# Kernel tuning notes

Hardware: AMD Instinct MI355X
Metric: run time of the kernel (lower is better)

The kernel has to match this reference:

```python
import jax, jax.numpy as jnp
import numpy as np

D = 64          # internal token dim (patch_encoder output)
E = 4           # num_experts
HID = 256       # expert hidden dim
NCLS = 10       # classifier output (hardcoded in source)


def gelu(x):
    return jax.nn.gelu(x, approximate=False)  # torch nn.GELU default = exact erf


def setup_inputs() -> dict:
    key = jax.random.key(0)
    ks = jax.random.split(key, 16)
    B, S, IN = 128, 1024, 192
    sc = lambda k, sh, fan: (jax.random.normal(k, sh, jnp.float32) / np.sqrt(fan))
    return {
        "x": jax.random.normal(ks[0], (B, S, IN), jnp.float32),
        # patch encoder: Linear(IN,64) -> GELU -> Linear(64,D)
        "pe_w1": sc(ks[1], (IN, 64), IN), "pe_b1": jnp.zeros((64,), jnp.float32),
        "pe_w2": sc(ks[2], (64, D), 64),  "pe_b2": jnp.zeros((D,), jnp.float32),
        # gate: Linear(D, E)
        "gate_w": sc(ks[3], (D, E), D), "gate_b": jnp.zeros((E,), jnp.float32),
        # experts: per-expert MLP D -> HID -> D
        "ew1": sc(ks[4], (E, D, HID), D), "eb1": jnp.zeros((E, HID), jnp.float32),
        "ew2": sc(ks[5], (E, HID, D), HID), "eb2": jnp.zeros((E, D), jnp.float32),
        # classifier: LayerNorm(D) -> Linear(D,D) -> GELU -> Linear(D,10)
        "ln_g": jnp.ones((D,), jnp.float32), "ln_b": jnp.zeros((D,), jnp.float32),
        "cl_w1": sc(ks[6], (D, D), D), "cl_b1": jnp.zeros((D,), jnp.float32),
        "cl_w2": sc(ks[7], (D, NCLS), D), "cl_b2": jnp.zeros((NCLS,), jnp.float32),
    }


def reference(x, pe_w1, pe_b1, pe_w2, pe_b2, gate_w, gate_b,
              ew1, eb1, ew2, eb2, ln_g, ln_b, cl_w1, cl_b1, cl_w2, cl_b2):
    # patch encoder: [B,S,IN] -> [B,S,D]
    h = gelu(x @ pe_w1 + pe_b1) @ pe_w2 + pe_b2

    # top-1 gating
    gate_logits = h @ gate_w + gate_b                      # [B,S,E]
    probs = jax.nn.softmax(gate_logits, axis=-1)
    top1 = jnp.argmax(probs, axis=-1)                      # [B,S] int
    onehot = jax.nn.one_hot(top1, E, dtype=h.dtype)        # [B,S,E] dispatch mask
    gate = jnp.sum(probs * onehot, axis=-1)                # [B,S] top-1 gate value

    # expert MLPs computed densely, combined by one-hot mask (same math as dispatch)
    eh = gelu(jnp.einsum('bsd,edh->bseh', h, ew1) + eb1)   # [B,S,E,HID]
    eo = jnp.einsum('bseh,ehd->bsed', eh, ew2) + eb2       # [B,S,E,D]
    moe_out = jnp.einsum('bsed,bse->bsd', eo, onehot) * gate[..., None]

    # switch-style load-balance aux loss: E * sum_e f_e * P_e
    f = jnp.mean(onehot, axis=(0, 1))                      # fraction routed per expert
    p = jnp.mean(probs, axis=(0, 1))                       # mean gate prob per expert
    aux_loss = E * jnp.sum(f * p)

    # mean pool over sequence, then classifier
    z = jnp.mean(moe_out, axis=1)                          # [B,D]
    mu = jnp.mean(z, axis=-1, keepdims=True)
    var = jnp.var(z, axis=-1, keepdims=True)
    zn = (z - mu) * jax.lax.rsqrt(var + 1e-5) * ln_g + ln_b
    y = gelu(zn @ cl_w1 + cl_b1) @ cl_w2 + cl_b2           # [B,10]
    return (y, aux_loss)
```

## Files before the change

kernel.cpp:

```cpp
#include <hip/hip_runtime.h>
#include <hip/hip_bf16.h>
#include <math.h>

typedef unsigned int  u32;
typedef unsigned short u16;
typedef unsigned long long u64;

using bf16x8  = __attribute__((ext_vector_type(8))) __bf16;
using float4v = __attribute__((ext_vector_type(4))) float;

#define MFMA16(a,b,c) __builtin_amdgcn_mfma_f32_16x16x32_bf16(a,b,c,0,0,0)

#define W1P_OFF   0u
#define W2P_OFF   24576u
#define GWP_OFF   40960u
#define E1P_OFF   43008u
#define E2P_OFF   174080u
#define ZF_OFF    305152u
#define CNTF_OFF  337920u
#define PSUMF_OFF 337984u
#define FAST_WS_BYTES 338048u

#define Z_OFF    0u
#define CNT_OFF  32768u
#define PSUM_OFF 32832u

__device__ inline u16 f2bf(float f){
  union { float f; u32 u; } v; v.f = f;
  u32 r = v.u + 0x7fffu + ((v.u >> 16) & 1u);
  return (u16)(r >> 16);
}
__device__ inline u32 pk2(float a, float b){
  union { __hip_bfloat162 h2; u32 u; } v;
  v.h2 = __float22bfloat162_rn(make_float2(a, b));
  return v.u;
}

__device__ inline float geluf(float x){
  float u = fabsf(x) * 0.70710678118654752f;
  float t = 1.0f / (1.0f + 0.3275911f * u);
  float poly = t*(0.254829592f + t*(-0.284496736f +
               t*(1.421413741f + t*(-1.453152027f + t*1.061405429f))));
  float er = 1.0f - poly * __expf(-u*u);
  return 0.5f * x * (1.0f + copysignf(er, x));
}

__global__ __launch_bounds__(256) void k0_pack(
    const float* __restrict__ w1, const float* __restrict__ w2, const float* __restrict__ gw,
    const float* __restrict__ e1, const float* __restrict__ e2,
    u16* w1p, u16* w2p, u16* gwp, u16* e1p, u16* e2p,
    float* z, u32* cnt, float* psum)
{
  int p = blockIdx.x*256 + threadIdx.x;
  if (p < 12288){
    int k = p >> 6, m = p & 63;
    int kc = k>>5, q = (k>>3)&3, j = k&7, mt = m>>4, col = m&15;
    w1p[((kc*4+mt)*64 + q*16+col)*8 + j] = f2bf(w1[p]); return;
  }
  p -= 12288;
  if (p < 4096){
    int k = p >> 6, m = p & 63;
    int kc = k>>5, q = (k>>3)&3, j = k&7, mt = m>>4, col = m&15;
    w2p[((kc*4+mt)*64 + q*16+col)*8 + j] = f2bf(w2[p]); return;
  }
  p -= 4096;
  if (p < 1024){
    int j = p & 7, lane = (p>>3) & 63;
    int col = lane & 15, q = lane >> 4, kc = p >> 9;
    int k = kc*32 + q*8 + j;
    gwp[p] = (col < 4) ? f2bf(gw[k*4 + col]) : (u16)0; return;
  }
  p -= 1024;
  if (p < 65536){
    int e = p >> 14, r = p & 16383;
    int k = r >> 8, m = r & 255;
    int kc = k>>5, q = (k>>3)&3, j = k&7, mt = m>>4, col = m&15;
    e1p[e*16384 + ((kc*16+mt)*64 + q*16+col)*8 + j] = f2bf(e1[p]); return;
  }
  p -= 65536;
  if (p < 65536){
    int e = p >> 14, r = p & 16383;
    int k = r >> 6, m = r & 63;
    int kc = k>>5, q = (k>>3)&3, j = k&7, mt = m>>4, col = m&15;
    e2p[e*16384 + ((kc*4+mt)*64 + q*16+col)*8 + j] = f2bf(e2[p]); return;
  }
  p -= 65536;
  if (p < 8192){ z[p] = 0.f; return; }
  p -= 8192;
  if (p < 4){ cnt[p] = 0u; return; }
  p -= 4;
  if (p < 4){ psum[p] = 0.f; return; }
}

__global__ __launch_bounds__(256) void kMain(
    const float* __restrict__ x,
    const float* __restrict__ b1, const float* __restrict__ b2, const float* __restrict__ gb,
    const u16* __restrict__ w1p, const u16* __restrict__ w2p, const u16* __restrict__ gwp,
    const u16* __restrict__ e1p, const u16* __restrict__ e2p,
    const float* __restrict__ eb1, const float* __restrict__ eb2,
    float* __restrict__ z, u32* __restrict__ cnt, float* __restrict__ psum)
{
  __shared__ char h1l[8192];
  __shared__ char hl[8192];
  __shared__ char hidp[8192];
  __shared__ int   be_s[64];
  __shared__ float gv_s[64];
  __shared__ int   sperm[64];
  __shared__ int   se_s[64];
  __shared__ float sg_s[64];
  __shared__ float lgp[4];
  __shared__ u32   lgc[4];

  const int tid  = threadIdx.x;
  const int tok0 = blockIdx.x * 64;
  if (tid < 4){ lgp[tid] = 0.f; lgc[tid] = 0u; }

  const int lane = tid & 63, wave = tid >> 6;
  const int col  = lane & 15, quad = lane >> 4;
  const int t    = wave*16 + col;

  bf16x8 bx[6];
  {
    const float* xrow = x + (size_t)(tok0 + t)*192 + quad*8;
    for (int kc = 0; kc < 6; ++kc){
      float4 f0 = *(const float4*)(xrow + kc*32);
      float4 f1 = *(const float4*)(xrow + kc*32 + 4);
      uint4 v;
      v.x = pk2(f0.x, f0.y); v.y = pk2(f0.z, f0.w);
      v.z = pk2(f1.x, f1.y); v.w = pk2(f1.z, f1.w);
      union { uint4 u; bf16x8 h; } cv; cv.u = v;
      bx[kc] = cv.h;
    }
  }

  for (int mt = 0; mt < 4; ++mt){
    float4v acc = {0.f,0.f,0.f,0.f};
    for (int kc = 0; kc < 6; ++kc){
      bf16x8 a = *(const bf16x8*)(w1p + ((kc*4 + mt)*64 + lane)*8);
      acc = MFMA16(a, bx[kc], acc);
    }
    int j0 = mt*16 + quad*4;
    float4 bb = *(const float4*)(b1 + j0);
    uint2 w; w.x = pk2(geluf(acc[0]+bb.x), geluf(acc[1]+bb.y));
             w.y = pk2(geluf(acc[2]+bb.z), geluf(acc[3]+bb.w));
    *(uint2*)(h1l + t*128 + (((2*mt + (quad>>1)) ^ (t & 7))*16) + (quad & 1)*8) = w;
  }

  {
    bf16x8 bh1[2];
    for (int kc = 0; kc < 2; ++kc)
      bh1[kc] = *(const bf16x8*)(h1l + t*128 + (((4*kc + quad) ^ (t & 7))*16));
    for (int mt = 0; mt < 4; ++mt){
      float4v acc = {0.f,0.f,0.f,0.f};
      for (int kc = 0; kc < 2; ++kc){
        bf16x8 a = *(const bf16x8*)(w2p + ((kc*4 + mt)*64 + lane)*8);
        acc = MFMA16(a, bh1[kc], acc);
      }
      int j0 = mt*16 + quad*4;
      float4 bb = *(const float4*)(b2 + j0);
      uint2 w; w.x = pk2(acc[0]+bb.x, acc[1]+bb.y);
               w.y = pk2(acc[2]+bb.z, acc[3]+bb.w);
      *(uint2*)(hl + t*128 + (((2*mt + (quad>>1)) ^ (t & 7))*16) + (quad & 1)*8) = w;
    }
  }

  {
    bf16x8 bh[2];
    for (int kc = 0; kc < 2; ++kc)
      bh[kc] = *(const bf16x8*)(hl + t*128 + (((4*kc + quad) ^ (t & 7))*16));
    float4v ag = {0.f,0.f,0.f,0.f};
    for (int kc = 0; kc < 2; ++kc){
      bf16x8 a = *(const bf16x8*)(gwp + (kc*64 + lane)*8);
      ag = MFMA16(a, bh[kc], ag);
    }
    if (quad == 0){
      float l0 = ag[0]+gb[0], l1 = ag[1]+gb[1], l2 = ag[2]+gb[2], l3 = ag[3]+gb[3];
      float mx = fmaxf(fmaxf(l0,l1), fmaxf(l2,l3));
      float x0 = __expf(l0-mx), x1 = __expf(l1-mx), x2 = __expf(l2-mx), x3 = __expf(l3-mx);
      float inv = 1.f/(x0+x1+x2+x3);
      float p0 = x0*inv, p1 = x1*inv, p2 = x2*inv, p3 = x3*inv;
      int be = 0; float bv = l0;
      if (l1 > bv){ bv = l1; be = 1; }
      if (l2 > bv){ bv = l2; be = 2; }
      if (l3 > bv){ bv = l3; be = 3; }
      be_s[t] = be;
      gv_s[t] = (be==0) ? p0 : (be==1) ? p1 : (be==2) ? p2 : p3;
      atomicAdd(&lgp[0], p0); atomicAdd(&lgp[1], p1);
      atomicAdd(&lgp[2], p2); atomicAdd(&lgp[3], p3);
      atomicAdd(&lgc[be], 1u);
    }
  }
  __syncthreads();

  if (tid < 64){
    int e = be_s[tid];
    u64 m0 = __ballot(e==0), m1 = __ballot(e==1), m2 = __ballot(e==2), m3 = __ballot(e==3);
    int c0 = __popcll(m0), c1 = __popcll(m1), c2 = __popcll(m2);
    int base = (e==0) ? 0 : (e==1) ? c0 : (e==2) ? c0+c1 : c0+c1+c2;
    u64 me = (e==0) ? m0 : (e==1) ? m1 : (e==2) ? m2 : m3;
    int pos = base + __popcll(me & ((1ull<<tid)-1ull));
    sperm[pos] = tid; se_s[pos] = e; sg_s[pos] = gv_s[tid];
  }
  __syncthreads();

  const int slice = wave*16;
  const int tt    = sperm[slice + col];
  const int myE   = se_s[slice + col];
  const float myG = sg_s[slice + col];
  const int e_lo  = se_s[slice], e_hi = se_s[slice + 15];
  char* hb = hidp + wave*2048;

  bf16x8 bhp[2];
  for (int kc = 0; kc < 2; ++kc)
    bhp[kc] = *(const bf16x8*)(hl + tt*128 + (((4*kc + quad) ^ (tt & 7))*16));

  float oacc[16];
  for (int i = 0; i < 16; ++i) oacc[i] = 0.f;

  for (int e = e_lo; e <= e_hi; ++e){
    const u16* W1 = e1p + e*16384;
    const u16* W2 = e2p + e*16384;
    float4v accE[4];
    for (int mt = 0; mt < 4; ++mt) accE[mt] = (float4v){0.f,0.f,0.f,0.f};
    for (int p = 0; p < 4; ++p){
      for (int mt2 = 0; mt2 < 4; ++mt2){
        float4v acc = {0.f,0.f,0.f,0.f};
        for (int kc = 0; kc < 2; ++kc){
          bf16x8 a = *(const bf16x8*)(W1 + ((kc*16 + p*4 + mt2)*64 + lane)*8);
          acc = MFMA16(a, bhp[kc], acc);
        }
        int j0 = p*64 + mt2*16 + quad*4;
        float4 bb = *(const float4*)(eb1 + e*256 + j0);
        uint2 w; w.x = pk2(geluf(acc[0]+bb.x), geluf(acc[1]+bb.y));
                 w.y = pk2(geluf(acc[2]+bb.z), geluf(acc[3]+bb.w));
        *(uint2*)(hb + col*128 + (((2*mt2 + (quad>>1)) ^ (col & 7))*16) + (quad & 1)*8) = w;
      }
      bf16x8 bhid0 = *(const bf16x8*)(hb + col*128 + (((0 + quad) ^ (col & 7))*16));
      bf16x8 bhid1 = *(const bf16x8*)(hb + col*128 + (((4 + quad) ^ (col & 7))*16));
      for (int mt = 0; mt < 4; ++mt){
        bf16x8 a0 = *(const bf16x8*)(W2 + (((p*2+0)*4 + mt)*64 + lane)*8);
        bf16x8 a1 = *(const bf16x8*)(W2 + (((p*2+1)*4 + mt)*64 + lane)*8);
        accE[mt] = MFMA16(a0, bhid0, accE[mt]);
        accE[mt] = MFMA16(a1, bhid1, accE[mt]);
      }
    }
    float wgt = (myE == e) ? myG : 0.f;
    for (int mt = 0; mt < 4; ++mt){
      float4 bb = *(const float4*)(eb2 + e*64 + mt*16 + quad*4);
      oacc[mt*4+0] += (accE[mt][0] + bb.x) * wgt;
      oacc[mt*4+1] += (accE[mt][1] + bb.y) * wgt;
      oacc[mt*4+2] += (accE[mt][2] + bb.z) * wgt;
      oacc[mt*4+3] += (accE[mt][3] + bb.w) * wgt;
    }
  }

  for (int m = 1; m < 16; m <<= 1)
    for (int i = 0; i < 16; ++i)
      oacc[i] += __shfl_xor(oacc[i], m, 64);
  if (col == 0){
    float* pw = (float*)hb;
    for (int mt = 0; mt < 4; ++mt)
      for (int r = 0; r < 4; ++r)
        pw[mt*16 + quad*4 + r] = oacc[mt*4 + r];
  }
  __syncthreads();
  int b = blockIdx.x >> 4;
  if (tid < 64){
    float s = ((const float*)(hidp))[tid]        + ((const float*)(hidp+2048))[tid]
            + ((const float*)(hidp+4096))[tid]   + ((const float*)(hidp+6144))[tid];
    atomicAdd(&z[b*64 + tid], s);
  }
  if (tid < 4){ atomicAdd(&cnt[tid], lgc[tid]); atomicAdd(&psum[tid], lgp[tid]); }
}

__global__ __launch_bounds__(64) void kFinal(
    const float* __restrict__ z, const u32* __restrict__ cnt, const float* __restrict__ psum,
    const float* __restrict__ ln_g, const float* __restrict__ ln_b,
    const float* __restrict__ cw1, const float* __restrict__ cb1,
    const float* __restrict__ cw2, const float* __restrict__ cb2,
    float* __restrict__ out)
{
  __shared__ float z_l[64], zn_l[64], c1_l[64], red[2];
  int tid = threadIdx.x, b = blockIdx.x;
  z_l[tid] = z[b*64 + tid] * (1.0f/1024.0f);
  __syncthreads();
  if (tid == 0){
    float mu = 0.f; for (int i=0;i<64;++i) mu += z_l[i]; mu *= (1.f/64.f);
    float vv = 0.f; for (int i=0;i<64;++i){ float d=z_l[i]-mu; vv += d*d; } vv *= (1.f/64.f);
    red[0]=mu; red[1]=1.0f/sqrtf(vv+1e-5f);
  }
  __syncthreads();
  zn_l[tid] = (z_l[tid]-red[0])*red[1]*ln_g[tid] + ln_b[tid];
  __syncthreads();
  float a1 = cb1[tid];
  for (int k=0;k<64;++k) a1 += zn_l[k]*cw1[k*64+tid];
  c1_l[tid] = geluf(a1);
  __syncthreads();
  if (tid < 10){
    float y = cb2[tid];
    for (int k=0;k<64;++k) y += c1_l[k]*cw2[k*10+tid];
    out[b*10+tid] = y;
  }
  if (b == 0 && tid == 0){
    float aux = 0.f;
    for (int e=0;e<4;++e) aux += (float)cnt[e]*psum[e];
    out[1280] = 4.0f*aux/(131072.0f*131072.0f);
  }
}

__global__ __launch_bounds__(256) void kInitF(float* z, u32* cnt, float* psum){
  int i = blockIdx.x*256 + threadIdx.x;
  if (i < 8192) z[i] = 0.f;
  if (i < 4){ cnt[i] = 0u; psum[i] = 0.f; }
}

__global__ __launch_bounds__(256) void kFusedF(
    const float* __restrict__ x,
    const float* __restrict__ w1, const float* __restrict__ b1,
    const float* __restrict__ w2, const float* __restrict__ b2,
    const float* __restrict__ gw, const float* __restrict__ gb,
    const float* __restrict__ e1, const float* __restrict__ eb1,
    const float* __restrict__ e2, const float* __restrict__ eb2,
    float* __restrict__ z, u32* __restrict__ cnt, float* __restrict__ psum)
{
  __shared__ float xs[4][192];
  __shared__ float h1s[4][64];
  __shared__ float hs[4][64];
  __shared__ float hid[4][256];
  __shared__ float lg[4][4];
  __shared__ int   be_s[4];
  __shared__ float gv_s[4];
  __shared__ float lgp[4];
  __shared__ u32   lgc[4];
  const int tid  = threadIdx.x;
  const int w    = tid >> 6, lane = tid & 63;
  const int tok  = blockIdx.x*4 + w;
  if (tid < 4){ lgp[tid] = 0.f; lgc[tid] = 0u; }
  for (int r = 0; r < 3; ++r)
    xs[w][lane + 64*r] = x[(size_t)tok*192 + lane + 64*r];
  __syncthreads();
  float a = b1[lane];
  for (int k = 0; k < 192; ++k) a += xs[w][k]*w1[k*64 + lane];
  h1s[w][lane] = geluf(a);
  __syncthreads();
  float h = b2[lane];
  for (int k = 0; k < 64; ++k) h += h1s[w][k]*w2[k*64 + lane];
  hs[w][lane] = h;
  __syncthreads();
  if (lane < 4){
    float l = gb[lane];
    for (int k = 0; k < 64; ++k) l += hs[w][k]*gw[k*4 + lane];
    lg[w][lane] = l;
  }
  __syncthreads();
  if (lane == 0){
    float l0=lg[w][0], l1=lg[w][1], l2=lg[w][2], l3=lg[w][3];
    float mx = fmaxf(fmaxf(l0,l1),fmaxf(l2,l3));
    float x0=expf(l0-mx), x1=expf(l1-mx), x2=expf(l2-mx), x3=expf(l3-mx);
    float inv = 1.f/(x0+x1+x2+x3);
    float p0=x0*inv, p1=x1*inv, p2=x2*inv, p3=x3*inv;
    int be=0; float bv=l0;
    if (l1>bv){bv=l1;be=1;}
    if (l2>bv){bv=l2;be=2;}
    if (l3>bv){bv=l3;be=3;}
    be_s[w]=be;
    gv_s[w]=(be==0)?p0:(be==1)?p1:(be==2)?p2:p3;
    atomicAdd(&lgp[0],p0); atomicAdd(&lgp[1],p1);
    atomicAdd(&lgp[2],p2); atomicAdd(&lgp[3],p3);
    atomicAdd(&lgc[be],1u);
  }
  __syncthreads();
  const int e    = be_s[w];
  const float gv = gv_s[w];
  const float* W1 = e1 + e*16384;
  const float* W2 = e2 + e*16384;
  for (int q = 0; q < 4; ++q){
    int j = q*64 + lane;
    float s = eb1[e*256 + j];
    for (int k = 0; k < 64; ++k) s += hs[w][k]*W1[k*256 + j];
    hid[w][j] = geluf(s);
  }
  __syncthreads();
  float o = eb2[e*64 + lane];
  for (int j = 0; j < 256; ++j) o += hid[w][j]*W2[j*64 + lane];
  int b = tok >> 10;
  atomicAdd(&z[b*64 + lane], o*gv);
  __syncthreads();
  if (tid < 4){ atomicAdd(&cnt[tid], lgc[tid]); atomicAdd(&psum[tid], lgp[tid]); }
}

extern "C" void kernel_launch(void* const* d_in, const int* in_sizes, int n_in,
                              void* d_out, int out_size, void* d_ws, size_t ws_size,
                              hipStream_t stream)
{
  const float* x    = (const float*)d_in[0];
  const float* pw1  = (const float*)d_in[1];
  const float* pb1  = (const float*)d_in[2];
  const float* pw2  = (const float*)d_in[3];
  const float* pb2  = (const float*)d_in[4];
  const float* gw   = (const float*)d_in[5];
  const float* gb   = (const float*)d_in[6];
  const float* ew1  = (const float*)d_in[7];
  const float* eb1  = (const float*)d_in[8];
  const float* ew2  = (const float*)d_in[9];
  const float* eb2  = (const float*)d_in[10];
  const float* lng  = (const float*)d_in[11];
  const float* lnb  = (const float*)d_in[12];
  const float* cw1  = (const float*)d_in[13];
  const float* cb1  = (const float*)d_in[14];
  const float* cw2  = (const float*)d_in[15];
  const float* cb2  = (const float*)d_in[16];
  char* ws  = (char*)d_ws;
  float* out = (float*)d_out;

  if (ws_size >= FAST_WS_BYTES){
    u16*  w1p  = (u16*)(ws + W1P_OFF);
    u16*  w2p  = (u16*)(ws + W2P_OFF);
    u16*  gwp  = (u16*)(ws + GWP_OFF);
    u16*  e1p  = (u16*)(ws + E1P_OFF);
    u16*  e2p  = (u16*)(ws + E2P_OFF);
    float* z    = (float*)(ws + ZF_OFF);
    u32*  cnt  = (u32*)(ws + CNTF_OFF);
    float* psum = (float*)(ws + PSUMF_OFF);
    k0_pack<<<613, 256, 0, stream>>>(pw1, pw2, gw, ew1, ew2,
                                     w1p, w2p, gwp, e1p, e2p, z, cnt, psum);
    kMain <<<2048, 256, 0, stream>>>(x, pb1, pb2, gb, w1p, w2p, gwp, e1p, e2p,
                                     eb1, eb2, z, cnt, psum);
    kFinal<<<128, 64, 0, stream>>>(z, cnt, psum, lng, lnb, cw1, cb1, cw2, cb2, out);
  } else {
    float* z    = (float*)(ws + Z_OFF);
    u32*   cnt  = (u32*)(ws + CNT_OFF);
    float* psum = (float*)(ws + PSUM_OFF);
    kInitF <<<32,    256, 0, stream>>>(z, cnt, psum);
    kFusedF<<<32768, 256, 0, stream>>>(x, pw1, pb1, pw2, pb2, gw, gb,
                                       ew1, eb1, ew2, eb2, z, cnt, psum);
    kFinal <<<128,   64,  0, stream>>>(z, cnt, psum, lng, lnb, cw1, cb1, cw2, cb2, out);
  }
}
```

Before: 292.4 us.

## Stage x loads through LDS coalesced, pad LDS rows, use fast reciprocals

Each wave now reads its 16 x rows with contiguous per-lane float4 loads, converts them to bf16, and stages them in a padded per-wave LDS region before gathering MFMA operands. The XOR-swizzled 128-byte LDS rows become 144-byte padded rows, and one per-wave scratch region is reused for h1, the expert hidden tile and the partial sums. Divisions in GELU and softmax use the hardware reciprocal, and the shared-memory atomics move after the barrier. The intent is better global load coalescing and cheaper arithmetic, at the cost of an extra LDS round trip and slightly less precise reciprocals.

```diff
diff --git a/kernel.cpp b/kernel.cpp
--- a/kernel.cpp
+++ b/kernel.cpp
@@ -38,7 +38,7 @@
 
 __device__ inline float geluf(float x){
   float u = fabsf(x) * 0.70710678118654752f;
-  float t = 1.0f / (1.0f + 0.3275911f * u);
+  float t = __builtin_amdgcn_rcpf(1.0f + 0.3275911f * u);
   float poly = t*(0.254829592f + t*(-0.284496736f +
                t*(1.421413741f + t*(-1.453152027f + t*1.061405429f))));
   float er = 1.0f - poly * __expf(-u*u);
@@ -100,9 +100,8 @@
     const float* __restrict__ eb1, const float* __restrict__ eb2,
     float* __restrict__ z, u32* __restrict__ cnt, float* __restrict__ psum)
 {
-  __shared__ char h1l[8192];
-  __shared__ char hl[8192];
-  __shared__ char hidp[8192];
+  __shared__ char wreg[25600];
+  __shared__ char hl[9216];
   __shared__ int   be_s[64];
   __shared__ float gv_s[64];
   __shared__ int   sperm[64];
@@ -112,27 +111,31 @@
   __shared__ u32   lgc[4];
 
   const int tid  = threadIdx.x;
-  const int tok0 = blockIdx.x * 64;
-  if (tid < 4){ lgp[tid] = 0.f; lgc[tid] = 0u; }
-
   const int lane = tid & 63, wave = tid >> 6;
   const int col  = lane & 15, quad = lane >> 4;
+  const int tok0 = blockIdx.x * 64;
   const int t    = wave*16 + col;
+  if (tid < 4){ lgp[tid] = 0.f; lgc[tid] = 0u; }
+
+  char* wr = wreg + wave*6400;
+
+  const float* xw = x + (size_t)(tok0 + wave*16)*192;
+  for (int it = 0; it < 6; ++it){
+    int task = it*64 + lane;
+    int tr = task / 24, c = task % 24;
+    float4 f0 = *(const float4*)(xw + tr*192 + c*8);
+    float4 f1 = *(const float4*)(xw + tr*192 + c*8 + 4);
+    uint4 v;
+    v.x = pk2(f0.x,f0.y); v.y = pk2(f0.z,f0.w);
+    v.z = pk2(f1.x,f1.y); v.w = pk2(f1.z,f1.w);
+    *(uint4*)(wr + tr*400 + c*16) = v;
+  }
 
   bf16x8 bx[6];
-  {
-    const float* xrow = x + (size_t)(tok0 + t)*192 + quad*8;
-    for (int kc = 0; kc < 6; ++kc){
-      float4 f0 = *(const float4*)(xrow + kc*32);
-      float4 f1 = *(const float4*)(xrow + kc*32 + 4);
-      uint4 v;
-      v.x = pk2(f0.x, f0.y); v.y = pk2(f0.z, f0.w);
-      v.z = pk2(f1.x, f1.y); v.w = pk2(f1.z, f1.w);
-      union { uint4 u; bf16x8 h; } cv; cv.u = v;
-      bx[kc] = cv.h;
-    }
-  }
-
+  for (int kc = 0; kc < 6; ++kc)
+    bx[kc] = *(const bf16x8*)(wr + col*400 + (4*kc+quad)*16);
+
+  char* h1t = wr;
   for (int mt = 0; mt < 4; ++mt){
     float4v acc = {0.f,0.f,0.f,0.f};
     for (int kc = 0; kc < 6; ++kc){
@@ -143,13 +146,13 @@
     float4 bb = *(const float4*)(b1 + j0);
     uint2 w; w.x = pk2(geluf(acc[0]+bb.x), geluf(acc[1]+bb.y));
              w.y = pk2(geluf(acc[2]+bb.z), geluf(acc[3]+bb.w));
-    *(uint2*)(h1l + t*128 + (((2*mt + (quad>>1)) ^ (t & 7))*16) + (quad & 1)*8) = w;
+    *(uint2*)(h1t + col*144 + mt*32 + quad*8) = w;
   }
 
   {
     bf16x8 bh1[2];
     for (int kc = 0; kc < 2; ++kc)
-      bh1[kc] = *(const bf16x8*)(h1l + t*128 + (((4*kc + quad) ^ (t & 7))*16));
+      bh1[kc] = *(const bf16x8*)(h1t + col*144 + (4*kc+quad)*16);
     for (int mt = 0; mt < 4; ++mt){
       float4v acc = {0.f,0.f,0.f,0.f};
       for (int kc = 0; kc < 2; ++kc){
@@ -160,14 +163,15 @@
       float4 bb = *(const float4*)(b2 + j0);
       uint2 w; w.x = pk2(acc[0]+bb.x, acc[1]+bb.y);
                w.y = pk2(acc[2]+bb.z, acc[3]+bb.w);
-      *(uint2*)(hl + t*128 + (((2*mt + (quad>>1)) ^ (t & 7))*16) + (quad & 1)*8) = w;
-    }
-  }
-
+      *(uint2*)(hl + t*144 + mt*32 + quad*8) = w;
+    }
+  }
+
+  float p0=0.f,p1=0.f,p2=0.f,p3=0.f; int be=0;
   {
     bf16x8 bh[2];
     for (int kc = 0; kc < 2; ++kc)
-      bh[kc] = *(const bf16x8*)(hl + t*128 + (((4*kc + quad) ^ (t & 7))*16));
+      bh[kc] = *(const bf16x8*)(hl + t*144 + (4*kc+quad)*16);
     float4v ag = {0.f,0.f,0.f,0.f};
     for (int kc = 0; kc < 2; ++kc){
       bf16x8 a = *(const bf16x8*)(gwp + (kc*64 + lane)*8);
@@ -177,20 +181,22 @@
       float l0 = ag[0]+gb[0], l1 = ag[1]+gb[1], l2 = ag[2]+gb[2], l3 = ag[3]+gb[3];
       float mx = fmaxf(fmaxf(l0,l1), fmaxf(l2,l3));
       float x0 = __expf(l0-mx), x1 = __expf(l1-mx), x2 = __expf(l2-mx), x3 = __expf(l3-mx);
-      float inv = 1.f/(x0+x1+x2+x3);
-      float p0 = x0*inv, p1 = x1*inv, p2 = x2*inv, p3 = x3*inv;
-      int be = 0; float bv = l0;
+      float inv = __builtin_amdgcn_rcpf(x0+x1+x2+x3);
+      p0 = x0*inv; p1 = x1*inv; p2 = x2*inv; p3 = x3*inv;
+      float bv = l0; be = 0;
       if (l1 > bv){ bv = l1; be = 1; }
       if (l2 > bv){ bv = l2; be = 2; }
       if (l3 > bv){ bv = l3; be = 3; }
       be_s[t] = be;
       gv_s[t] = (be==0) ? p0 : (be==1) ? p1 : (be==2) ? p2 : p3;
-      atomicAdd(&lgp[0], p0); atomicAdd(&lgp[1], p1);
-      atomicAdd(&lgp[2], p2); atomicAdd(&lgp[3], p3);
-      atomicAdd(&lgc[be], 1u);
-    }
-  }
-  __syncthreads();
+    }
+  }
+  __syncthreads();
+  if (quad == 0){
+    atomicAdd(&lgp[0], p0); atomicAdd(&lgp[1], p1);
+    atomicAdd(&lgp[2], p2); atomicAdd(&lgp[3], p3);
+    atomicAdd(&lgc[be], 1u);
+  }
 
   if (tid < 64){
     int e = be_s[tid];
@@ -208,11 +214,11 @@
   const int myE   = se_s[slice + col];
   const float myG = sg_s[slice + col];
   const int e_lo  = se_s[slice], e_hi = se_s[slice + 15];
-  char* hb = hidp + wave*2048;
+  char* hbt = wr;
 
   bf16x8 bhp[2];
   for (int kc = 0; kc < 2; ++kc)
-    bhp[kc] = *(const bf16x8*)(hl + tt*128 + (((4*kc + quad) ^ (tt & 7))*16));
+    bhp[kc] = *(const bf16x8*)(hl + tt*144 + (4*kc+quad)*16);
 
   float oacc[16];
   for (int i = 0; i < 16; ++i) oacc[i] = 0.f;
@@ -233,15 +239,15 @@
         float4 bb = *(const float4*)(eb1 + e*256 + j0);
         uint2 w; w.x = pk2(geluf(acc[0]+bb.x), geluf(acc[1]+bb.y));
                  w.y = pk2(geluf(acc[2]+bb.z), geluf(acc[3]+bb.w));
-        *(uint2*)(hb + col*128 + (((2*mt2 + (quad>>1)) ^ (col & 7))*16) + (quad & 1)*8) = w;
+        *(uint2*)(hbt + col*144 + mt2*32 + quad*8) = w;
       }
-      bf16x8 bhid0 = *(const bf16x8*)(hb + col*128 + (((0 + quad) ^ (col & 7))*16));
-      bf16x8 bhid1 = *(const bf16x8*)(hb + col*128 + (((4 + quad) ^ (col & 7))*16));
+      bf16x8 bq0 = *(const bf16x8*)(hbt + col*144 + quad*16);
+      bf16x8 bq1 = *(const bf16x8*)(hbt + col*144 + (4+quad)*16);
       for (int mt = 0; mt < 4; ++mt){
         bf16x8 a0 = *(const bf16x8*)(W2 + (((p*2+0)*4 + mt)*64 + lane)*8);
         bf16x8 a1 = *(const bf16x8*)(W2 + (((p*2+1)*4 + mt)*64 + lane)*8);
-        accE[mt] = MFMA16(a0, bhid0, accE[mt]);
-        accE[mt] = MFMA16(a1, bhid1, accE[mt]);
+        accE[mt] = MFMA16(a0, bq0, accE[mt]);
+        accE[mt] = MFMA16(a1, bq1, accE[mt]);
       }
     }
     float wgt = (myE == e) ? myG : 0.f;
@@ -258,7 +264,7 @@
     for (int i = 0; i < 16; ++i)
       oacc[i] += __shfl_xor(oacc[i], m, 64);
   if (col == 0){
-    float* pw = (float*)hb;
+    float* pw = (float*)wr;
     for (int mt = 0; mt < 4; ++mt)
       for (int r = 0; r < 4; ++r)
         pw[mt*16 + quad*4 + r] = oacc[mt*4 + r];
@@ -266,8 +272,8 @@
   __syncthreads();
   int b = blockIdx.x >> 4;
   if (tid < 64){
-    float s = ((const float*)(hidp))[tid]        + ((const float*)(hidp+2048))[tid]
-            + ((const float*)(hidp+4096))[tid]   + ((const float*)(hidp+6144))[tid];
+    float s = *(const float*)(wreg + tid*4)         + *(const float*)(wreg + 6400 + tid*4)
+            + *(const float*)(wreg + 12800 + tid*4) + *(const float*)(wreg + 19200 + tid*4);
     atomicAdd(&z[b*64 + tid], s);
   }
   if (tid < 4){ atomicAdd(&cnt[tid], lgc[tid]); atomicAdd(&psum[tid], lgp[tid]); }
```

New measurement: 271.0 us. 7.3% less time.
